# Performance work log

Measured on AMD Instinct MI355X. Metric: run time of the kernel, lower is better.

Reference implementation:

```python
import jax, jax.numpy as jnp
import numpy as np

N_NODES = 50000
N_EDGES = 600000
N_FEAT = 128
N_DIMS = 128
N_CLSS = 10


def setup_inputs() -> dict:
    key = jax.random.key(0)
    ks = jax.random.split(key, 9)
    x = jax.random.normal(ks[0], (N_NODES, N_FEAT), dtype=jnp.float32)
    edge_index = jax.random.randint(ks[1], (2, N_EDGES), 0, N_NODES, dtype=jnp.int32)
    edge_weight = jax.random.uniform(ks[2], (N_EDGES,), dtype=jnp.float32)
    # Glorot-ish init for learned params
    W1 = jax.random.normal(ks[3], (N_FEAT, N_DIMS), dtype=jnp.float32) * (1.0 / np.sqrt(N_FEAT))
    b1 = jnp.zeros((N_DIMS,), dtype=jnp.float32)
    W2 = jax.random.normal(ks[4], (N_DIMS, N_DIMS), dtype=jnp.float32) * (1.0 / np.sqrt(N_DIMS))
    b2 = jnp.zeros((N_DIMS,), dtype=jnp.float32)
    Wc = jax.random.normal(ks[5], (N_DIMS, N_CLSS), dtype=jnp.float32) * (1.0 / np.sqrt(N_DIMS))
    bc = jnp.zeros((N_CLSS,), dtype=jnp.float32)
    return {"x": x, "edge_index": edge_index, "edge_weight": edge_weight,
            "W1": W1, "b1": b1, "W2": W2, "b2": b2, "Wc": Wc, "bc": bc}


def gcn_conv(x, W, b, src, dst, ew, n_nodes):
    """PyG GCNConv (add_self_loops=True, improved=False, bias=True).
    out[i] = sum_{(j->i) in E} d_i^-1/2 * w_ji * d_j^-1/2 * (xW)[j]
             + d_i^-1 * (xW)[i]  (self loop, weight 1) + b
    where d_i = 1 + sum of incoming edge weights at i.
    """
    h = x @ W                                                   # [N, D]
    deg = jax.ops.segment_sum(ew, dst, num_segments=n_nodes) + 1.0  # self-loop weight 1
    dinv = jax.lax.rsqrt(deg)                                   # deg >= 1, no inf
    norm = dinv[src] * ew * dinv[dst]                           # [E]
    agg = jax.ops.segment_sum(h[src] * norm[:, None], dst, num_segments=n_nodes)
    agg = agg + h * (dinv * dinv)[:, None]                      # self-loop term
    return agg + b


def reference(x, edge_index, edge_weight, W1, b1, W2, b2, Wc, bc):
    n = x.shape[0]
    src, dst = edge_index[0], edge_index[1]
    h = jax.nn.relu(gcn_conv(x, W1, b1, src, dst, edge_weight, n))
    # dropout is identity in eval mode
    h = gcn_conv(h, W2, b2, src, dst, edge_weight, n)
    h = jax.nn.relu(h)
    return h @ Wc + bc
```

## Files before the change

### kernel.cpp

```cpp
#include <hip/hip_runtime.h>
#include <hip/hip_bf16.h>

#define N_NODES 50000
#define N_EDGES 600000
#define NC 10
#define GB ((N_NODES + 63) / 64)

typedef __attribute__((ext_vector_type(8))) __bf16 bf16x8;
typedef __attribute__((ext_vector_type(8))) unsigned short u16x8;
typedef __attribute__((ext_vector_type(4))) float f32x4;

__device__ __forceinline__ unsigned short f2bf(float f) {
    unsigned u = __float_as_uint(f);
    u += 0x7fff + ((u >> 16) & 1);
    return (unsigned short)(u >> 16);
}
__device__ __forceinline__ int rfl(int x) { return __builtin_amdgcn_readfirstlane(x); }
__device__ __forceinline__ float rflf(float x) {
    return __uint_as_float(__builtin_amdgcn_readfirstlane(__float_as_uint(x)));
}

__global__ void k_zero(int4* __restrict__ p, int n4) {
    int i = blockIdx.x * blockDim.x + threadIdx.x;
    if (i < n4) p[i] = make_int4(0, 0, 0, 0);
}

__global__ void k_prep(const float* __restrict__ W1, const float* __restrict__ W2,
                       unsigned short* __restrict__ wt1, unsigned short* __restrict__ wt2,
                       const int4* __restrict__ dst4, int* __restrict__ cnt,
                       int4* __restrict__ ord4) {
    int b = blockIdx.x;
    if (b < 128) {
        const float* W = (b < 64) ? W1 : W2;
        unsigned short* Wt = (b < 64) ? wt1 : wt2;
        int i = (b & 63) * 256 + threadIdx.x;
        int n = i >> 7, k = i & 127;
        Wt[n * 128 + k] = f2bf(W[k * 128 + n]);
    } else {
        int i = (b - 128) * 256 + threadIdx.x;
        if (i < N_EDGES / 4) {
            int4 d = dst4[i];
            int4 o;
            o.x = atomicAdd(&cnt[d.x], 1);
            o.y = atomicAdd(&cnt[d.y], 1);
            o.z = atomicAdd(&cnt[d.z], 1);
            o.w = atomicAdd(&cnt[d.w], 1);
            ord4[i] = o;
        }
    }
}

__global__ void k_scan1(const int* __restrict__ cnt, int* __restrict__ rowptr,
                        int* __restrict__ bsum, int n) {
    __shared__ int sh[256];
    int t = threadIdx.x;
    int i = blockIdx.x * 256 + t;
    int v = (i < n) ? cnt[i] : 0;
    sh[t] = v;
    __syncthreads();
    for (int off = 1; off < 256; off <<= 1) {
        int x = 0;
        if (t >= off) x = sh[t - off];
        __syncthreads();
        sh[t] += x;
        __syncthreads();
    }
    if (i < n) rowptr[i] = sh[t] - v;
    if (t == 255) bsum[blockIdx.x] = sh[255];
}

__global__ void k_scan2(int* __restrict__ bsum, int nb) {
    __shared__ int sh[256];
    int t = threadIdx.x;
    int v = (t < nb) ? bsum[t] : 0;
    sh[t] = v;
    __syncthreads();
    for (int off = 1; off < 256; off <<= 1) {
        int x = 0;
        if (t >= off) x = sh[t - off];
        __syncthreads();
        sh[t] += x;
        __syncthreads();
    }
    if (t < nb) bsum[t] = sh[t] - v;
}

__global__ void k_scan3(int* __restrict__ rowptr, const int* __restrict__ bsum, int n) {
    int t = threadIdx.x;
    int i = blockIdx.x * 256 + t;
    if (i < n) rowptr[i] += bsum[blockIdx.x];
    if (blockIdx.x == 0 && t == 0) rowptr[n] = N_EDGES;
}

template <int FP32IN>
__device__ __forceinline__ void gemm_body(unsigned short* Al, unsigned short* Bl,
                                          const void* __restrict__ Xin,
                                          const unsigned short* __restrict__ Wt,
                                          unsigned short* __restrict__ Yb,
                                          int M, int row0) {
    int t = threadIdx.x;
    for (int i = t; i < 2048; i += 256) {
        int r = i >> 4, q = i & 15;
        *(u16x8*)(Bl + r * 128 + ((q ^ (r & 7)) << 3)) =
            *(const u16x8*)(Wt + r * 128 + (q << 3));
    }
    for (int i = t; i < 1024; i += 256) {
        int r = i >> 4, q = i & 15;
        int gr = row0 + r;
        u16x8 v;
        if (FP32IN) {
            const float* X = (const float*)Xin;
            if (gr < M) {
                float4 f0 = *(const float4*)(X + (size_t)gr * 128 + (q << 3));
                float4 f1 = *(const float4*)(X + (size_t)gr * 128 + (q << 3) + 4);
                v[0] = f2bf(f0.x); v[1] = f2bf(f0.y); v[2] = f2bf(f0.z); v[3] = f2bf(f0.w);
                v[4] = f2bf(f1.x); v[5] = f2bf(f1.y); v[6] = f2bf(f1.z); v[7] = f2bf(f1.w);
            } else {
#pragma unroll
                for (int j = 0; j < 8; ++j) v[j] = 0;
            }
        } else {
            const unsigned short* X = (const unsigned short*)Xin;
            if (gr < M) {
                v = *(const u16x8*)(X + (size_t)gr * 128 + (q << 3));
            } else {
#pragma unroll
                for (int j = 0; j < 8; ++j) v[j] = 0;
            }
        }
        *(u16x8*)(Al + r * 128 + ((q ^ (r & 7)) << 3)) = v;
    }
    __syncthreads();

    int l  = t & 63;
    int w  = t >> 6;
    int ar = (w << 4) + (l & 15);
    int kq = l >> 4;

    bf16x8 af[4];
#pragma unroll
    for (int s = 0; s < 4; ++s) {
        int g = ((s << 2) + kq) ^ (l & 7);
        af[s] = *(const bf16x8*)(Al + ar * 128 + (g << 3));
    }

    f32x4 acc[8];
#pragma unroll
    for (int c = 0; c < 8; ++c)
#pragma unroll
        for (int j = 0; j < 4; ++j) acc[c][j] = 0.0f;

#pragma unroll
    for (int c = 0; c < 8; ++c) {
        int br = (c << 4) + (l & 15);
#pragma unroll
        for (int s = 0; s < 4; ++s) {
            int g = ((s << 2) + kq) ^ (l & 7);
            bf16x8 bf = *(const bf16x8*)(Bl + br * 128 + (g << 3));
            acc[c] = __builtin_amdgcn_mfma_f32_16x16x32_bf16(af[s], bf, acc[c], 0, 0, 0);
        }
    }

    int orow = row0 + (w << 4) + ((l >> 4) << 2);
    int ocol = l & 15;
#pragma unroll
    for (int c = 0; c < 8; ++c) {
#pragma unroll
        for (int j = 0; j < 4; ++j) {
            int r = orow + j;
            if (r < M) Yb[(size_t)r * 128 + (c << 4) + ocol] = f2bf(acc[c][j]);
        }
    }
}

__global__ __launch_bounds__(256) void k_sg(const float* __restrict__ X,
                                            const unsigned short* __restrict__ Wt,
                                            unsigned short* __restrict__ Yb, int M,
                                            const int* __restrict__ src,
                                            const int* __restrict__ dst,
                                            const float* __restrict__ ew,
                                            const int* __restrict__ ord,
                                            const int* __restrict__ rowptr,
                                            int* __restrict__ esrc,
                                            float* __restrict__ ew2) {
    __shared__ unsigned short Al[64 * 128];
    __shared__ unsigned short Bl[128 * 128];
    if (blockIdx.x < GB) {
        gemm_body<1>(Al, Bl, X, Wt, Yb, M, blockIdx.x * 64);
    } else {
        int e = (blockIdx.x - GB) * 256 + threadIdx.x;
        if (e < N_EDGES) {
            int pos = rowptr[dst[e]] + ord[e];
            esrc[pos] = src[e];
            ew2[pos]  = ew[e];
        }
    }
}

__global__ void k_deg(const int* __restrict__ rowptr, const float* __restrict__ ew2,
                      float* __restrict__ dinv) {
    int i = blockIdx.x * blockDim.x + threadIdx.x;
    if (i >= N_NODES) return;
    int p1 = rowptr[i + 1];
    float s = 1.0f;
    for (int p = rowptr[i]; p < p1; ++p) s += ew2[p];
    dinv[i] = rsqrtf(s);
}

__global__ void k_norm(const int* __restrict__ rowptr, const int* __restrict__ esrc,
                       const float* __restrict__ ew2, const float* __restrict__ dinv,
                       float* __restrict__ enorm) {
    int i = blockIdx.x * blockDim.x + threadIdx.x;
    if (i >= N_NODES) return;
    float di = dinv[i];
    int p  = rowptr[i];
    int p1 = rowptr[i + 1];
    for (; p + 4 <= p1; p += 4) {
        int s0 = esrc[p], s1 = esrc[p+1], s2 = esrc[p+2], s3 = esrc[p+3];
        float d0 = dinv[s0], d1 = dinv[s1], d2 = dinv[s2], d3 = dinv[s3];
        enorm[p]   = d0 * ew2[p]   * di;
        enorm[p+1] = d1 * ew2[p+1] * di;
        enorm[p+2] = d2 * ew2[p+2] * di;
        enorm[p+3] = d3 * ew2[p+3] * di;
    }
    for (; p < p1; ++p) enorm[p] = dinv[esrc[p]] * ew2[p] * di;
}

__device__ __forceinline__ float2 agg_row(const unsigned* __restrict__ hb,
                                          const int* __restrict__ rowptr,
                                          const int* __restrict__ esrc,
                                          const float* __restrict__ enorm,
                                          const float* __restrict__ dinv,
                                          int node, int lane) {
    int p  = rfl(rowptr[node]);
    int p1 = rfl(rowptr[node + 1]);
    float di  = dinv[node];
    float di2 = di * di;
    unsigned sv = hb[(size_t)node * 64 + lane];
    float2 acc;
    acc.x = __uint_as_float(sv << 16) * di2;
    acc.y = __uint_as_float(sv & 0xffff0000u) * di2;

    while (p + 16 <= p1) {
        int s[16]; float w[16]; unsigned v[16];
#pragma unroll
        for (int i = 0; i < 16; ++i) {
            s[i] = rfl(esrc[p + i]);
            w[i] = rflf(enorm[p + i]);
        }
#pragma unroll
        for (int i = 0; i < 16; ++i) v[i] = hb[(size_t)s[i] * 64 + lane];
#pragma unroll
        for (int i = 0; i < 16; ++i) {
            acc.x += w[i] * __uint_as_float(v[i] << 16);
            acc.y += w[i] * __uint_as_float(v[i] & 0xffff0000u);
        }
        p += 16;
    }
    while (p + 4 <= p1) {
        int s[4]; float w[4]; unsigned v[4];
#pragma unroll
        for (int i = 0; i < 4; ++i) {
            s[i] = rfl(esrc[p + i]);
            w[i] = rflf(enorm[p + i]);
        }
#pragma unroll
        for (int i = 0; i < 4; ++i) v[i] = hb[(size_t)s[i] * 64 + lane];
#pragma unroll
        for (int i = 0; i < 4; ++i) {
            acc.x += w[i] * __uint_as_float(v[i] << 16);
            acc.y += w[i] * __uint_as_float(v[i] & 0xffff0000u);
        }
        p += 4;
    }
    for (; p < p1; ++p) {
        int s = rfl(esrc[p]);
        float w = rflf(enorm[p]);
        unsigned v = hb[(size_t)s * 64 + lane];
        acc.x += w * __uint_as_float(v << 16);
        acc.y += w * __uint_as_float(v & 0xffff0000u);
    }
    return acc;
}

__global__ __launch_bounds__(256) void k_ag(const unsigned* __restrict__ hb,
                                            const int* __restrict__ rowptr,
                                            const int* __restrict__ esrc,
                                            const float* __restrict__ enorm,
                                            const float* __restrict__ dinv,
                                            const float* __restrict__ bias,
                                            const unsigned short* __restrict__ Wt,
                                            unsigned short* __restrict__ Yb, int M) {
    __shared__ unsigned short Al[64 * 128];
    int t = threadIdx.x;
    int l = t & 63;
    int w = t >> 6;
    int row0 = blockIdx.x * 64;

    for (int nd = 0; nd < 16; ++nd) {
        int r = (w << 4) + nd;
        int node = row0 + r;
        float2 acc = make_float2(0.f, 0.f);
        if (node < M) {
            acc = agg_row(hb, rowptr, esrc, enorm, dinv, node, l);
            float2 bv = ((const float2*)bias)[l];
            acc.x = fmaxf(acc.x + bv.x, 0.f);
            acc.y = fmaxf(acc.y + bv.y, 0.f);
        }
        unsigned val = f2bf(acc.x) | ((unsigned)f2bf(acc.y) << 16);
        int q = l >> 2;
        *(unsigned*)(Al + r * 128 + ((q ^ (r & 7)) << 3) + ((l & 3) << 1)) = val;
    }
    __syncthreads();

    int ar = (w << 4) + (l & 15);
    int kq = l >> 4;
    bf16x8 af[4];
#pragma unroll
    for (int s = 0; s < 4; ++s) {
        int g = ((s << 2) + kq) ^ (ar & 7);
        af[s] = *(const bf16x8*)(Al + ar * 128 + (g << 3));
    }

    f32x4 acc2[8];
#pragma unroll
    for (int c = 0; c < 8; ++c)
#pragma unroll
        for (int j = 0; j < 4; ++j) acc2[c][j] = 0.0f;

#pragma unroll
    for (int c = 0; c < 8; ++c) {
        int br = (c << 4) + (l & 15);
#pragma unroll
        for (int s = 0; s < 4; ++s) {
            bf16x8 bf = *(const bf16x8*)(Wt + br * 128 + (((s << 2) + kq) << 3));
            acc2[c] = __builtin_amdgcn_mfma_f32_16x16x32_bf16(af[s], bf, acc2[c], 0, 0, 0);
        }
    }

    int orow = row0 + (w << 4) + ((l >> 4) << 2);
    int ocol = l & 15;
#pragma unroll
    for (int c = 0; c < 8; ++c) {
#pragma unroll
        for (int j = 0; j < 4; ++j) {
            int r = orow + j;
            if (r < M) Yb[(size_t)r * 128 + (c << 4) + ocol] = f2bf(acc2[c][j]);
        }
    }
}

__global__ __launch_bounds__(256) void k_agg(const unsigned* __restrict__ hb,
                                             const int* __restrict__ rowptr,
                                             const int* __restrict__ esrc,
                                             const float* __restrict__ enorm,
                                             const float* __restrict__ dinv,
                                             const float* __restrict__ bias,
                                             const float* __restrict__ Wc,
                                             const float* __restrict__ bc,
                                             float* __restrict__ out) {
    int wid  = (blockIdx.x * blockDim.x + threadIdx.x) >> 6;
    int lane = threadIdx.x & 63;
    if (wid >= N_NODES) return;
    wid = rfl(wid);
    float2 acc = agg_row(hb, rowptr, esrc, enorm, dinv, wid, lane);
    float2 bv = ((const float2*)bias)[lane];
    acc.x = fmaxf(acc.x + bv.x, 0.f);
    acc.y = fmaxf(acc.y + bv.y, 0.f);

    int k0 = 2 * lane;
    float r[NC];
#pragma unroll
    for (int c = 0; c < NC; ++c)
        r[c] = acc.x * Wc[k0 * NC + c] + acc.y * Wc[(k0 + 1) * NC + c];
#pragma unroll
    for (int off = 32; off; off >>= 1)
#pragma unroll
        for (int c = 0; c < NC; ++c)
            r[c] += __shfl_xor(r[c], off, 64);
    if (lane < NC) out[(size_t)wid * NC + lane] = r[lane] + bc[lane];
}

extern "C" void kernel_launch(void* const* d_in, const int* in_sizes, int n_in,
                              void* d_out, int out_size, void* d_ws, size_t ws_size,
                              hipStream_t stream) {
    const float* x   = (const float*)d_in[0];
    const int*   ei  = (const int*)d_in[1];
    const float* ew  = (const float*)d_in[2];
    const float* W1  = (const float*)d_in[3];
    const float* b1  = (const float*)d_in[4];
    const float* W2  = (const float*)d_in[5];
    const float* b2  = (const float*)d_in[6];
    const float* Wc  = (const float*)d_in[7];
    const float* bc  = (const float*)d_in[8];
    float*       out = (float*)d_out;

    const int* src = ei;
    const int* dst = ei + N_EDGES;

    size_t off = 0;
    auto carve = [&](size_t bytes) {
        void* p = (char*)d_ws + off;
        off += (bytes + 255) & ~(size_t)255;
        return p;
    };
    unsigned short* hb  = (unsigned short*)carve((size_t)N_NODES * 128 * 2);
    unsigned short* hb2 = (unsigned short*)carve((size_t)N_NODES * 128 * 2);
    unsigned short* wt1 = (unsigned short*)carve(128 * 128 * 2);
    unsigned short* wt2 = (unsigned short*)carve(128 * 128 * 2);
    float* dinv   = (float*)carve((size_t)N_NODES * 4);
    int*   cnt    = (int*)carve((size_t)N_NODES * 4);
    int*   rowptr = (int*)carve((size_t)(N_NODES + 1) * 4);
    int*   bsum   = (int*)carve(256 * 4);
    int*   ord    = (int*)carve((size_t)N_EDGES * 4);
    int*   esrc   = (int*)carve((size_t)N_EDGES * 4);
    float* ew2    = (float*)carve((size_t)N_EDGES * 4);
    float* enorm  = (float*)carve((size_t)N_EDGES * 4);
    (void)ws_size; (void)n_in; (void)in_sizes; (void)out_size;

    int nb = (N_NODES + 255) / 256;
    int eb = (N_EDGES + 255) / 256;

    k_zero<<<(N_NODES / 4 + 255) / 256, 256, 0, stream>>>((int4*)cnt, N_NODES / 4);
    k_prep<<<128 + (N_EDGES / 4 + 255) / 256, 256, 0, stream>>>(
        W1, W2, wt1, wt2, (const int4*)dst, cnt, (int4*)ord);
    k_scan1<<<nb, 256, 0, stream>>>(cnt, rowptr, bsum, N_NODES);
    k_scan2<<<1, 256, 0, stream>>>(bsum, nb);
    k_scan3<<<nb, 256, 0, stream>>>(rowptr, bsum, N_NODES);
    k_sg<<<GB + eb, 256, 0, stream>>>(x, wt1, hb, N_NODES,
                                      src, dst, ew, ord, rowptr, esrc, ew2);
    k_deg<<<nb, 256, 0, stream>>>(rowptr, ew2, dinv);
    k_norm<<<nb, 256, 0, stream>>>(rowptr, esrc, ew2, dinv, enorm);

    k_ag<<<GB, 256, 0, stream>>>((const unsigned*)hb, rowptr, esrc, enorm, dinv,
                                 b1, wt2, hb2, N_NODES);
    k_agg<<<(N_NODES + 3) / 4, 256, 0, stream>>>((const unsigned*)hb2, rowptr, esrc,
                                                 enorm, dinv, b2, Wc, bc, out);
}
```

Measured before the change: 173.8 us.

## Split layer-1 aggregation from GEMM2 and overlap tail aggregation with GEMM

The fused aggregate-then-GEMM kernel, which ran 16 serial row aggregations per wave before its MFMA phase, is replaced by a one-wave-per-node aggregation kernel that writes an intermediate bf16 buffer. A mixed kernel then aggregates the remaining 10000 nodes while other blocks run GEMM2 on the first 40000 rows, and a small kernel finishes GEMM2 on the tail. Separately, the second and third scan kernels are merged into one, which recomputes the block-sum scan in every block. The split adds an extra 12.8 MB write and read of the intermediate and two more launches, in exchange for better latency hiding during aggregation.

```diff
diff --git a/kernel.cpp b/kernel.cpp
--- a/kernel.cpp
+++ b/kernel.cpp
@@ -5,6 +5,10 @@
 #define N_EDGES 600000
 #define NC 10
 #define GB ((N_NODES + 63) / 64)
+#define NSPLIT 40000
+#define AGGB2 ((N_NODES - NSPLIT) / 4)
+#define GEMA  (NSPLIT / 64)
+#define GEMB  ((N_NODES - NSPLIT + 63) / 64 + 1)
 
 typedef __attribute__((ext_vector_type(8))) __bf16 bf16x8;
 typedef __attribute__((ext_vector_type(8))) unsigned short u16x8;
@@ -69,8 +73,10 @@
     if (t == 255) bsum[blockIdx.x] = sh[255];
 }
 
-__global__ void k_scan2(int* __restrict__ bsum, int nb) {
+__global__ void k_scan23(int* __restrict__ rowptr, const int* __restrict__ bsum,
+                         int nb, int n) {
     __shared__ int sh[256];
+    __shared__ int ex[256];
     int t = threadIdx.x;
     int v = (t < nb) ? bsum[t] : 0;
     sh[t] = v;
@@ -82,13 +88,10 @@
         sh[t] += x;
         __syncthreads();
     }
-    if (t < nb) bsum[t] = sh[t] - v;
-}
-
-__global__ void k_scan3(int* __restrict__ rowptr, const int* __restrict__ bsum, int n) {
-    int t = threadIdx.x;
+    ex[t] = sh[t] - v;
+    __syncthreads();
     int i = blockIdx.x * 256 + t;
-    if (i < n) rowptr[i] += bsum[blockIdx.x];
+    if (i < n) rowptr[i] += ex[blockIdx.x];
     if (blockIdx.x == 0 && t == 0) rowptr[n] = N_EDGES;
 }
 
@@ -157,6 +160,66 @@
         for (int s = 0; s < 4; ++s) {
             int g = ((s << 2) + kq) ^ (l & 7);
             bf16x8 bf = *(const bf16x8*)(Bl + br * 128 + (g << 3));
+            acc[c] = __builtin_amdgcn_mfma_f32_16x16x32_bf16(af[s], bf, acc[c], 0, 0, 0);
+        }
+    }
+
+    int orow = row0 + (w << 4) + ((l >> 4) << 2);
+    int ocol = l & 15;
+#pragma unroll
+    for (int c = 0; c < 8; ++c) {
+#pragma unroll
+        for (int j = 0; j < 4; ++j) {
+            int r = orow + j;
+            if (r < M) Yb[(size_t)r * 128 + (c << 4) + ocol] = f2bf(acc[c][j]);
+        }
+    }
+}
+
+__device__ __forceinline__ void gemm_lite(unsigned short* Al,
+                                          const unsigned short* __restrict__ Xb,
+                                          const unsigned short* __restrict__ Wt,
+                                          unsigned short* __restrict__ Yb,
+                                          int M, int row0) {
+    int t = threadIdx.x;
+    for (int i = t; i < 1024; i += 256) {
+        int r = i >> 4, q = i & 15;
+        int gr = row0 + r;
+        u16x8 v;
+        if (gr < M) {
+            v = *(const u16x8*)(Xb + (size_t)gr * 128 + (q << 3));
+        } else {
+#pragma unroll
+            for (int j = 0; j < 8; ++j) v[j] = 0;
+        }
+        *(u16x8*)(Al + r * 128 + ((q ^ (r & 7)) << 3)) = v;
+    }
+    __syncthreads();
+
+    int l  = t & 63;
+    int w  = t >> 6;
+    int ar = (w << 4) + (l & 15);
+    int kq = l >> 4;
+
+    bf16x8 af[4];
+#pragma unroll
+    for (int s = 0; s < 4; ++s) {
+        int g = ((s << 2) + kq) ^ (l & 7);
+        af[s] = *(const bf16x8*)(Al + ar * 128 + (g << 3));
+    }
+
+    f32x4 acc[8];
+#pragma unroll
+    for (int c = 0; c < 8; ++c)
+#pragma unroll
+        for (int j = 0; j < 4; ++j) acc[c][j] = 0.0f;
+
+#pragma unroll
+    for (int c = 0; c < 8; ++c) {
+        int br = (c << 4) + (l & 15);
+#pragma unroll
+        for (int s = 0; s < 4; ++s) {
+            bf16x8 bf = *(const bf16x8*)(Wt + br * 128 + (((s << 2) + kq) << 3));
             acc[c] = __builtin_amdgcn_mfma_f32_16x16x32_bf16(af[s], bf, acc[c], 0, 0, 0);
         }
     }
@@ -283,82 +346,68 @@
     return acc;
 }
 
-__global__ __launch_bounds__(256) void k_ag(const unsigned* __restrict__ hb,
+__global__ __launch_bounds__(256) void k_agg0(const unsigned* __restrict__ hb,
+                                              const int* __restrict__ rowptr,
+                                              const int* __restrict__ esrc,
+                                              const float* __restrict__ enorm,
+                                              const float* __restrict__ dinv,
+                                              const float* __restrict__ bias,
+                                              unsigned* __restrict__ outb, int node0) {
+    int wid  = node0 + ((blockIdx.x * blockDim.x + threadIdx.x) >> 6);
+    int lane = threadIdx.x & 63;
+    if (wid >= N_NODES) return;
+    wid = rfl(wid);
+    float2 acc = agg_row(hb, rowptr, esrc, enorm, dinv, wid, lane);
+    float2 bv = ((const float2*)bias)[lane];
+    acc.x = fmaxf(acc.x + bv.x, 0.f);
+    acc.y = fmaxf(acc.y + bv.y, 0.f);
+    outb[(size_t)wid * 64 + lane] = f2bf(acc.x) | ((unsigned)f2bf(acc.y) << 16);
+}
+
+__global__ __launch_bounds__(256) void k_gx(const unsigned* __restrict__ hb,
                                             const int* __restrict__ rowptr,
                                             const int* __restrict__ esrc,
                                             const float* __restrict__ enorm,
                                             const float* __restrict__ dinv,
                                             const float* __restrict__ bias,
-                                            const unsigned short* __restrict__ Wt,
-                                            unsigned short* __restrict__ Yb, int M) {
+                                            unsigned* __restrict__ zb,
+                                            const unsigned short* __restrict__ zread,
+                                            const unsigned short* __restrict__ wt2,
+                                            unsigned short* __restrict__ hb2) {
     __shared__ unsigned short Al[64 * 128];
-    int t = threadIdx.x;
-    int l = t & 63;
-    int w = t >> 6;
-    int row0 = blockIdx.x * 64;
-
-    for (int nd = 0; nd < 16; ++nd) {
-        int r = (w << 4) + nd;
-        int node = row0 + r;
-        float2 acc = make_float2(0.f, 0.f);
-        if (node < M) {
-            acc = agg_row(hb, rowptr, esrc, enorm, dinv, node, l);
-            float2 bv = ((const float2*)bias)[l];
-            acc.x = fmaxf(acc.x + bv.x, 0.f);
-            acc.y = fmaxf(acc.y + bv.y, 0.f);
-        }
-        unsigned val = f2bf(acc.x) | ((unsigned)f2bf(acc.y) << 16);
-        int q = l >> 2;
-        *(unsigned*)(Al + r * 128 + ((q ^ (r & 7)) << 3) + ((l & 3) << 1)) = val;
-    }
-    __syncthreads();
-
-    int ar = (w << 4) + (l & 15);
-    int kq = l >> 4;
-    bf16x8 af[4];
-#pragma unroll
-    for (int s = 0; s < 4; ++s) {
-        int g = ((s << 2) + kq) ^ (ar & 7);
-        af[s] = *(const bf16x8*)(Al + ar * 128 + (g << 3));
-    }
-
-    f32x4 acc2[8];
-#pragma unroll
-    for (int c = 0; c < 8; ++c)
-#pragma unroll
-        for (int j = 0; j < 4; ++j) acc2[c][j] = 0.0f;
-
-#pragma unroll
-    for (int c = 0; c < 8; ++c) {
-        int br = (c << 4) + (l & 15);
-#pragma unroll
-        for (int s = 0; s < 4; ++s) {
-            bf16x8 bf = *(const bf16x8*)(Wt + br * 128 + (((s << 2) + kq) << 3));
-            acc2[c] = __builtin_amdgcn_mfma_f32_16x16x32_bf16(af[s], bf, acc2[c], 0, 0, 0);
-        }
-    }
-
-    int orow = row0 + (w << 4) + ((l >> 4) << 2);
-    int ocol = l & 15;
-#pragma unroll
-    for (int c = 0; c < 8; ++c) {
-#pragma unroll
-        for (int j = 0; j < 4; ++j) {
-            int r = orow + j;
-            if (r < M) Yb[(size_t)r * 128 + (c << 4) + ocol] = f2bf(acc2[c][j]);
-        }
-    }
-}
-
-__global__ __launch_bounds__(256) void k_agg(const unsigned* __restrict__ hb,
-                                             const int* __restrict__ rowptr,
-                                             const int* __restrict__ esrc,
-                                             const float* __restrict__ enorm,
-                                             const float* __restrict__ dinv,
-                                             const float* __restrict__ bias,
-                                             const float* __restrict__ Wc,
-                                             const float* __restrict__ bc,
-                                             float* __restrict__ out) {
+    if (blockIdx.x < AGGB2) {
+        int wid  = NSPLIT + ((blockIdx.x * blockDim.x + threadIdx.x) >> 6);
+        int lane = threadIdx.x & 63;
+        if (wid >= N_NODES) return;
+        wid = rfl(wid);
+        float2 acc = agg_row(hb, rowptr, esrc, enorm, dinv, wid, lane);
+        float2 bv = ((const float2*)bias)[lane];
+        acc.x = fmaxf(acc.x + bv.x, 0.f);
+        acc.y = fmaxf(acc.y + bv.y, 0.f);
+        zb[(size_t)wid * 64 + lane] = f2bf(acc.x) | ((unsigned)f2bf(acc.y) << 16);
+    } else {
+        int row0 = (blockIdx.x - AGGB2) * 64;
+        gemm_lite(Al, zread, wt2, hb2, NSPLIT, row0);
+    }
+}
+
+__global__ __launch_bounds__(256) void k_gemm2b(const unsigned short* __restrict__ zread,
+                                                const unsigned short* __restrict__ wt2,
+                                                unsigned short* __restrict__ hb2) {
+    __shared__ unsigned short Al[64 * 128];
+    int row0 = NSPLIT + blockIdx.x * 64;
+    gemm_lite(Al, zread, wt2, hb2, N_NODES, row0);
+}
+
+__global__ __launch_bounds__(256) void k_agg1(const unsigned* __restrict__ hb,
+                                              const int* __restrict__ rowptr,
+                                              const int* __restrict__ esrc,
+                                              const float* __restrict__ enorm,
+                                              const float* __restrict__ dinv,
+                                              const float* __restrict__ bias,
+                                              const float* __restrict__ Wc,
+                                              const float* __restrict__ bc,
+                                              float* __restrict__ out) {
     int wid  = (blockIdx.x * blockDim.x + threadIdx.x) >> 6;
     int lane = threadIdx.x & 63;
     if (wid >= N_NODES) return;
@@ -405,6 +454,7 @@
         return p;
     };
     unsigned short* hb  = (unsigned short*)carve((size_t)N_NODES * 128 * 2);
+    unsigned short* zb  = (unsigned short*)carve((size_t)N_NODES * 128 * 2);
     unsigned short* hb2 = (unsigned short*)carve((size_t)N_NODES * 128 * 2);
     unsigned short* wt1 = (unsigned short*)carve(128 * 128 * 2);
     unsigned short* wt2 = (unsigned short*)carve(128 * 128 * 2);
@@ -425,15 +475,18 @@
     k_prep<<<128 + (N_EDGES / 4 + 255) / 256, 256, 0, stream>>>(
         W1, W2, wt1, wt2, (const int4*)dst, cnt, (int4*)ord);
     k_scan1<<<nb, 256, 0, stream>>>(cnt, rowptr, bsum, N_NODES);
-    k_scan2<<<1, 256, 0, stream>>>(bsum, nb);
-    k_scan3<<<nb, 256, 0, stream>>>(rowptr, bsum, N_NODES);
+    k_scan23<<<nb, 256, 0, stream>>>(rowptr, bsum, nb, N_NODES);
     k_sg<<<GB + eb, 256, 0, stream>>>(x, wt1, hb, N_NODES,
                                       src, dst, ew, ord, rowptr, esrc, ew2);
     k_deg<<<nb, 256, 0, stream>>>(rowptr, ew2, dinv);
     k_norm<<<nb, 256, 0, stream>>>(rowptr, esrc, ew2, dinv, enorm);
 
-    k_ag<<<GB, 256, 0, stream>>>((const unsigned*)hb, rowptr, esrc, enorm, dinv,
-                                 b1, wt2, hb2, N_NODES);
-    k_agg<<<(N_NODES + 3) / 4, 256, 0, stream>>>((const unsigned*)hb2, rowptr, esrc,
-                                                 enorm, dinv, b2, Wc, bc, out);
-}
+    k_agg0<<<NSPLIT / 4, 256, 0, stream>>>((const unsigned*)hb, rowptr, esrc,
+                                           enorm, dinv, b1, (unsigned*)zb, 0);
+    k_gx<<<AGGB2 + GEMA, 256, 0, stream>>>((const unsigned*)hb, rowptr, esrc,
+                                           enorm, dinv, b1, (unsigned*)zb,
+                                           zb, wt2, hb2);
+    k_gemm2b<<<GEMB, 256, 0, stream>>>(zb, wt2, hb2);
+    k_agg1<<<(N_NODES + 3) / 4, 256, 0, stream>>>((const unsigned*)hb2, rowptr, esrc,
+                                                  enorm, dinv, b2, Wc, bc, out);
+}
```

Result: faster. 169.8 us (-2.3%).
